# Kernel optimization log

Measured on AMD Instinct MI355X. Metric: run time of the kernel, lower is better.

Reference implementation:

```python
import jax, jax.numpy as jnp
import numpy as np

EPS = 1e-10


def setup_inputs() -> dict:
    key = jax.random.key(0)
    k1, k2 = jax.random.split(key)
    b, p, c = 8192, 512, 1000
    x = jax.random.normal(k1, (b, p), dtype=jnp.float32)
    means = jax.random.normal(k2, (c, p), dtype=jnp.float32)
    return {"x": x, "means": means}


def reference(x, means):
    # scale factor: L2 norm of the first class mean (np.linalg.norm(mean_logits_np[0]))
    scale = jnp.sqrt(jnp.sum(means[0] ** 2))
    # L2-normalize x along feature dim, then rescale to ||means[0]||
    xn = x / (jnp.linalg.norm(x, axis=1, keepdims=True) + EPS) * scale
    # logits = -||xn - mu_c||^2, expanded as -(||xn||^2 - 2 xn.mu + ||mu||^2)
    # avoids materializing the (b, num_classes, p) intermediate of the original
    x_sq = jnp.sum(xn * xn, axis=1, keepdims=True)          # (b, 1)
    m_sq = jnp.sum(means * means, axis=1)                   # (c,)
    cross = jnp.einsum('bp,cp->bc', xn, means)              # (b, c)
    logits = -(x_sq - 2.0 * cross + m_sq[None, :])
    return logits
```

## Files before the change

### kernel.cpp

```cpp
#include <hip/hip_runtime.h>
#include <hip/hip_bf16.h>
#include <stdint.h>

typedef __bf16 bf16x8 __attribute__((ext_vector_type(8)));
typedef float  f32x4  __attribute__((ext_vector_type(4)));
typedef __attribute__((address_space(1))) const void* gptr_t;
typedef __attribute__((address_space(3))) void*       sptr_t;

#define B_ROWS 8192
#define C_CLS  1000
#define C_PAD  1024
#define P_DIM  512
#define EPS    1e-10f

#define WS_MEANS_BF 0
#define WS_MSQ      1048576
#define WS_XN_BF    1052672
#define WS_XSQ      9441280

__global__ __launch_bounds__(64) void prep_means_k(const float* __restrict__ means,
                                                   __hip_bfloat16* __restrict__ means_bf,
                                                   float* __restrict__ m_sq) {
    const int c = blockIdx.x;
    const int l = threadIdx.x;
    if (c < C_CLS) {
        const float4* mr = (const float4*)(means + (size_t)c * P_DIM);
        float4 a = mr[l * 2];
        float4 b = mr[l * 2 + 1];
        float s = a.x * a.x + a.y * a.y + a.z * a.z + a.w * a.w
                + b.x * b.x + b.y * b.y + b.z * b.z + b.w * b.w;
        alignas(16) __hip_bfloat16 tmp[8];
        tmp[0] = __float2bfloat16(a.x); tmp[1] = __float2bfloat16(a.y);
        tmp[2] = __float2bfloat16(a.z); tmp[3] = __float2bfloat16(a.w);
        tmp[4] = __float2bfloat16(b.x); tmp[5] = __float2bfloat16(b.y);
        tmp[6] = __float2bfloat16(b.z); tmp[7] = __float2bfloat16(b.w);
        *(uint4*)(means_bf + (size_t)c * P_DIM + l * 8) = *(const uint4*)tmp;
        #pragma unroll
        for (int off = 32; off > 0; off >>= 1) s += __shfl_down(s, off);
        if (l == 0) m_sq[c] = s;
    } else {
        uint4 z = {0u, 0u, 0u, 0u};
        *(uint4*)(means_bf + (size_t)c * P_DIM + l * 8) = z;
        if (l == 0) m_sq[c] = 0.0f;
    }
}

__global__ __launch_bounds__(256) void prep_x_k(const float* __restrict__ x,
                                                const float* __restrict__ m_sq,
                                                __hip_bfloat16* __restrict__ xn_bf,
                                                float* __restrict__ x_sq) {
    const int w = threadIdx.x >> 6;
    const int l = threadIdx.x & 63;
    const int row = blockIdx.x * 4 + w;
    const float4* xr = (const float4*)(x + (size_t)row * P_DIM);
    float4 a = xr[l * 2];
    float4 b = xr[l * 2 + 1];
    float s = a.x * a.x + a.y * a.y + a.z * a.z + a.w * a.w
            + b.x * b.x + b.y * b.y + b.z * b.z + b.w * b.w;
    #pragma unroll
    for (int off = 32; off > 0; off >>= 1) s += __shfl_down(s, off);
    s = __shfl(s, 0);
    float norm  = sqrtf(s);
    float scale = sqrtf(m_sq[0]);
    float sc    = scale / (norm + EPS);
    alignas(16) __hip_bfloat16 tmp[8];
    tmp[0] = __float2bfloat16(a.x * sc); tmp[1] = __float2bfloat16(a.y * sc);
    tmp[2] = __float2bfloat16(a.z * sc); tmp[3] = __float2bfloat16(a.w * sc);
    tmp[4] = __float2bfloat16(b.x * sc); tmp[5] = __float2bfloat16(b.y * sc);
    tmp[6] = __float2bfloat16(b.z * sc); tmp[7] = __float2bfloat16(b.w * sc);
    *(uint4*)(xn_bf + (size_t)row * P_DIM + l * 8) = *(const uint4*)tmp;
    if (l == 0) {
        float sn = sc * norm;
        x_sq[row] = sn * sn;
    }
}

__global__ __launch_bounds__(256) void gemm_k(const __hip_bfloat16* __restrict__ A,
                                              const __hip_bfloat16* __restrict__ B,
                                              const float* __restrict__ x_sq,
                                              const float* __restrict__ m_sq,
                                              float* __restrict__ out) {
    __shared__ alignas(16) char lds[16384];
    const int t  = threadIdx.x;
    const int w  = t >> 6;
    const int l  = t & 63;
    const int wr = w >> 1;
    const int wc = w & 1;
    const int q   = l >> 4;
    const int m16 = l & 15;

    const int brow = blockIdx.y;
    const int bcol = blockIdx.x;

    f32x4 acc[4][4];
    #pragma unroll
    for (int i = 0; i < 4; ++i)
        #pragma unroll
        for (int j = 0; j < 4; ++j) {
            f32x4 z = {0.f, 0.f, 0.f, 0.f};
            acc[i][j] = z;
        }

    const char* Abase = (const char*)A + (size_t)(brow * 128) * (P_DIM * 2);
    const char* Bbase = (const char*)B + (size_t)(bcol * 128) * (P_DIM * 2);

    for (int k0 = 0; k0 < P_DIM; k0 += 32) {
        #pragma unroll
        for (int r = 0; r < 2; ++r) {
            const int o    = r * 4096 + t * 16;
            const int trow = o >> 6;
            const int kb   = o & 63;
            const char* gA = Abase + (size_t)trow * (P_DIM * 2) + k0 * 2 + kb;
            const char* gB = Bbase + (size_t)trow * (P_DIM * 2) + k0 * 2 + kb;
            char* dA = lds + r * 4096 + w * 1024;
            char* dB = lds + 8192 + r * 4096 + w * 1024;
            __builtin_amdgcn_global_load_lds((gptr_t)gA, (sptr_t)dA, 16, 0, 0);
            __builtin_amdgcn_global_load_lds((gptr_t)gB, (sptr_t)dB, 16, 0, 0);
        }
        __syncthreads();

        bf16x8 af[4], bfr[4];
        #pragma unroll
        for (int i = 0; i < 4; ++i) {
            const int m = wr * 64 + i * 16 + m16;
            af[i] = *(const bf16x8*)(lds + m * 64 + q * 16);
        }
        #pragma unroll
        for (int j = 0; j < 4; ++j) {
            const int n = wc * 64 + j * 16 + m16;
            bfr[j] = *(const bf16x8*)(lds + 8192 + n * 64 + q * 16);
        }
        #pragma unroll
        for (int i = 0; i < 4; ++i)
            #pragma unroll
            for (int j = 0; j < 4; ++j)
                acc[i][j] = __builtin_amdgcn_mfma_f32_16x16x32_bf16(af[i], bfr[j], acc[i][j], 0, 0, 0);
        __syncthreads();
    }

    const int rowbase = brow * 128 + wr * 64;
    const int colbase = bcol * 128 + wc * 64;
    float msq[4];
    #pragma unroll
    for (int j = 0; j < 4; ++j) {
        const int col = colbase + j * 16 + m16;
        msq[j] = (col < C_CLS) ? m_sq[col] : 0.0f;
    }
    #pragma unroll
    for (int i = 0; i < 4; ++i) {
        #pragma unroll
        for (int reg = 0; reg < 4; ++reg) {
            const int row = rowbase + i * 16 + q * 4 + reg;
            const float xsq = x_sq[row];
            #pragma unroll
            for (int j = 0; j < 4; ++j) {
                const int col = colbase + j * 16 + m16;
                if (col < C_CLS) {
                    out[(size_t)row * C_CLS + col] = 2.0f * acc[i][j][reg] - xsq - msq[j];
                }
            }
        }
    }
}

extern "C" void kernel_launch(void* const* d_in, const int* in_sizes, int n_in,
                              void* d_out, int out_size, void* d_ws, size_t ws_size,
                              hipStream_t stream) {
    const float* x     = (const float*)d_in[0];
    const float* means = (const float*)d_in[1];
    float* out = (float*)d_out;
    char* ws = (char*)d_ws;

    __hip_bfloat16* means_bf = (__hip_bfloat16*)(ws + WS_MEANS_BF);
    float*          m_sq     = (float*)(ws + WS_MSQ);
    __hip_bfloat16* xn_bf    = (__hip_bfloat16*)(ws + WS_XN_BF);
    float*          x_sq     = (float*)(ws + WS_XSQ);

    prep_means_k<<<C_PAD, 64, 0, stream>>>(means, means_bf, m_sq);
    prep_x_k<<<B_ROWS / 4, 256, 0, stream>>>(x, m_sq, xn_bf, x_sq);
    gemm_k<<<dim3(C_PAD / 128, B_ROWS / 128), 256, 0, stream>>>(xn_bf, means_bf, x_sq, m_sq, out);
}
```

Before: 98.28 us.

## Merge prep kernels and shrink GEMM tile to 64x128 for more blocks

Merges the two preprocessing kernels into one launch. Each x-row block recomputes the norm of means[0] itself, which removes the dependency on m_sq from the means pass. The GEMM tile shrinks from 128x128 to 64x128 with four waves each owning 64x32, and launch bounds request 4 blocks per CU, doubling the grid to 1024 blocks for better occupancy on the many-CU GPU. The cost is lower per-block data reuse (A tile shared over fewer columns) and redundant means[0] loads in every prep block.

```diff
diff --git a/kernel.cpp b/kernel.cpp
--- a/kernel.cpp
+++ b/kernel.cpp
@@ -18,131 +18,142 @@
 #define WS_XN_BF    1052672
 #define WS_XSQ      9441280
 
-__global__ __launch_bounds__(64) void prep_means_k(const float* __restrict__ means,
-                                                   __hip_bfloat16* __restrict__ means_bf,
-                                                   float* __restrict__ m_sq) {
-    const int c = blockIdx.x;
-    const int l = threadIdx.x;
-    if (c < C_CLS) {
-        const float4* mr = (const float4*)(means + (size_t)c * P_DIM);
-        float4 a = mr[l * 2];
-        float4 b = mr[l * 2 + 1];
-        float s = a.x * a.x + a.y * a.y + a.z * a.z + a.w * a.w
-                + b.x * b.x + b.y * b.y + b.z * b.z + b.w * b.w;
+__device__ __forceinline__ float dot8(float4 a, float4 b) {
+    return a.x * a.x + a.y * a.y + a.z * a.z + a.w * a.w
+         + b.x * b.x + b.y * b.y + b.z * b.z + b.w * b.w;
+}
+
+__global__ __launch_bounds__(256) void prep_k(const float* __restrict__ x,
+                                              const float* __restrict__ means,
+                                              __hip_bfloat16* __restrict__ means_bf,
+                                              float* __restrict__ m_sq,
+                                              __hip_bfloat16* __restrict__ xn_bf,
+                                              float* __restrict__ x_sq) {
+    const int w = threadIdx.x >> 6;
+    const int l = threadIdx.x & 63;
+    const int bid = blockIdx.x;
+
+    if (bid < B_ROWS / 4) {
+        const int row = bid * 4 + w;
+        const float4* m0 = (const float4*)means;
+        float4 ma = m0[l * 2];
+        float4 mb = m0[l * 2 + 1];
+        float ms = dot8(ma, mb);
+        const float4* xr = (const float4*)(x + (size_t)row * P_DIM);
+        float4 a = xr[l * 2];
+        float4 b = xr[l * 2 + 1];
+        float s = dot8(a, b);
+        #pragma unroll
+        for (int off = 32; off > 0; off >>= 1) {
+            ms += __shfl_down(ms, off);
+            s  += __shfl_down(s, off);
+        }
+        ms = __shfl(ms, 0);
+        s  = __shfl(s, 0);
+        float scale = sqrtf(ms);
+        float norm  = sqrtf(s);
+        float sc    = scale / (norm + EPS);
         alignas(16) __hip_bfloat16 tmp[8];
-        tmp[0] = __float2bfloat16(a.x); tmp[1] = __float2bfloat16(a.y);
-        tmp[2] = __float2bfloat16(a.z); tmp[3] = __float2bfloat16(a.w);
-        tmp[4] = __float2bfloat16(b.x); tmp[5] = __float2bfloat16(b.y);
-        tmp[6] = __float2bfloat16(b.z); tmp[7] = __float2bfloat16(b.w);
-        *(uint4*)(means_bf + (size_t)c * P_DIM + l * 8) = *(const uint4*)tmp;
-        #pragma unroll
-        for (int off = 32; off > 0; off >>= 1) s += __shfl_down(s, off);
-        if (l == 0) m_sq[c] = s;
+        tmp[0] = __float2bfloat16(a.x * sc); tmp[1] = __float2bfloat16(a.y * sc);
+        tmp[2] = __float2bfloat16(a.z * sc); tmp[3] = __float2bfloat16(a.w * sc);
+        tmp[4] = __float2bfloat16(b.x * sc); tmp[5] = __float2bfloat16(b.y * sc);
+        tmp[6] = __float2bfloat16(b.z * sc); tmp[7] = __float2bfloat16(b.w * sc);
+        *(uint4*)(xn_bf + (size_t)row * P_DIM + l * 8) = *(const uint4*)tmp;
+        if (l == 0) {
+            float sn = sc * norm;
+            x_sq[row] = sn * sn;
+        }
     } else {
-        uint4 z = {0u, 0u, 0u, 0u};
-        *(uint4*)(means_bf + (size_t)c * P_DIM + l * 8) = z;
-        if (l == 0) m_sq[c] = 0.0f;
+        const int c = (bid - B_ROWS / 4) * 4 + w;
+        if (c < C_CLS) {
+            const float4* mr = (const float4*)(means + (size_t)c * P_DIM);
+            float4 a = mr[l * 2];
+            float4 b = mr[l * 2 + 1];
+            float s = dot8(a, b);
+            alignas(16) __hip_bfloat16 tmp[8];
+            tmp[0] = __float2bfloat16(a.x); tmp[1] = __float2bfloat16(a.y);
+            tmp[2] = __float2bfloat16(a.z); tmp[3] = __float2bfloat16(a.w);
+            tmp[4] = __float2bfloat16(b.x); tmp[5] = __float2bfloat16(b.y);
+            tmp[6] = __float2bfloat16(b.z); tmp[7] = __float2bfloat16(b.w);
+            *(uint4*)(means_bf + (size_t)c * P_DIM + l * 8) = *(const uint4*)tmp;
+            #pragma unroll
+            for (int off = 32; off > 0; off >>= 1) s += __shfl_down(s, off);
+            if (l == 0) m_sq[c] = s;
+        } else {
+            uint4 z = {0u, 0u, 0u, 0u};
+            *(uint4*)(means_bf + (size_t)c * P_DIM + l * 8) = z;
+            if (l == 0) m_sq[c] = 0.0f;
+        }
     }
 }
 
-__global__ __launch_bounds__(256) void prep_x_k(const float* __restrict__ x,
-                                                const float* __restrict__ m_sq,
-                                                __hip_bfloat16* __restrict__ xn_bf,
-                                                float* __restrict__ x_sq) {
-    const int w = threadIdx.x >> 6;
-    const int l = threadIdx.x & 63;
-    const int row = blockIdx.x * 4 + w;
-    const float4* xr = (const float4*)(x + (size_t)row * P_DIM);
-    float4 a = xr[l * 2];
-    float4 b = xr[l * 2 + 1];
-    float s = a.x * a.x + a.y * a.y + a.z * a.z + a.w * a.w
-            + b.x * b.x + b.y * b.y + b.z * b.z + b.w * b.w;
-    #pragma unroll
-    for (int off = 32; off > 0; off >>= 1) s += __shfl_down(s, off);
-    s = __shfl(s, 0);
-    float norm  = sqrtf(s);
-    float scale = sqrtf(m_sq[0]);
-    float sc    = scale / (norm + EPS);
-    alignas(16) __hip_bfloat16 tmp[8];
-    tmp[0] = __float2bfloat16(a.x * sc); tmp[1] = __float2bfloat16(a.y * sc);
-    tmp[2] = __float2bfloat16(a.z * sc); tmp[3] = __float2bfloat16(a.w * sc);
-    tmp[4] = __float2bfloat16(b.x * sc); tmp[5] = __float2bfloat16(b.y * sc);
-    tmp[6] = __float2bfloat16(b.z * sc); tmp[7] = __float2bfloat16(b.w * sc);
-    *(uint4*)(xn_bf + (size_t)row * P_DIM + l * 8) = *(const uint4*)tmp;
-    if (l == 0) {
-        float sn = sc * norm;
-        x_sq[row] = sn * sn;
-    }
-}
-
-__global__ __launch_bounds__(256) void gemm_k(const __hip_bfloat16* __restrict__ A,
-                                              const __hip_bfloat16* __restrict__ B,
-                                              const float* __restrict__ x_sq,
-                                              const float* __restrict__ m_sq,
-                                              float* __restrict__ out) {
-    __shared__ alignas(16) char lds[16384];
-    const int t  = threadIdx.x;
-    const int w  = t >> 6;
-    const int l  = t & 63;
-    const int wr = w >> 1;
-    const int wc = w & 1;
+__global__ __launch_bounds__(256, 4) void gemm_k(const __hip_bfloat16* __restrict__ A,
+                                                 const __hip_bfloat16* __restrict__ B,
+                                                 const float* __restrict__ x_sq,
+                                                 const float* __restrict__ m_sq,
+                                                 float* __restrict__ out) {
+    __shared__ alignas(16) char lds[12288];
+    const int t   = threadIdx.x;
+    const int w   = t >> 6;
+    const int l   = t & 63;
     const int q   = l >> 4;
     const int m16 = l & 15;
 
     const int brow = blockIdx.y;
     const int bcol = blockIdx.x;
 
-    f32x4 acc[4][4];
+    f32x4 acc[4][2];
     #pragma unroll
     for (int i = 0; i < 4; ++i)
         #pragma unroll
-        for (int j = 0; j < 4; ++j) {
+        for (int j = 0; j < 2; ++j) {
             f32x4 z = {0.f, 0.f, 0.f, 0.f};
             acc[i][j] = z;
         }
 
-    const char* Abase = (const char*)A + (size_t)(brow * 128) * (P_DIM * 2);
+    const char* Abase = (const char*)A + (size_t)(brow * 64)  * (P_DIM * 2);
     const char* Bbase = (const char*)B + (size_t)(bcol * 128) * (P_DIM * 2);
 
     for (int k0 = 0; k0 < P_DIM; k0 += 32) {
         #pragma unroll
-        for (int r = 0; r < 2; ++r) {
-            const int o    = r * 4096 + t * 16;
-            const int trow = o >> 6;
-            const int kb   = o & 63;
-            const char* gA = Abase + (size_t)trow * (P_DIM * 2) + k0 * 2 + kb;
-            const char* gB = Bbase + (size_t)trow * (P_DIM * 2) + k0 * 2 + kb;
-            char* dA = lds + r * 4096 + w * 1024;
-            char* dB = lds + 8192 + r * 4096 + w * 1024;
-            __builtin_amdgcn_global_load_lds((gptr_t)gA, (sptr_t)dA, 16, 0, 0);
-            __builtin_amdgcn_global_load_lds((gptr_t)gB, (sptr_t)dB, 16, 0, 0);
+        for (int r = 0; r < 3; ++r) {
+            const int wbase = r * 4096 + w * 1024;
+            const int o     = wbase + l * 16;
+            const char* g;
+            if (r == 0) {
+                g = Abase + (size_t)(o >> 6) * (P_DIM * 2) + k0 * 2 + (o & 63);
+            } else {
+                const int o2 = o - 4096;
+                g = Bbase + (size_t)(o2 >> 6) * (P_DIM * 2) + k0 * 2 + (o2 & 63);
+            }
+            __builtin_amdgcn_global_load_lds((gptr_t)g, (sptr_t)(lds + wbase), 16, 0, 0);
         }
         __syncthreads();
 
-        bf16x8 af[4], bfr[4];
+        bf16x8 af[4], bfr[2];
         #pragma unroll
         for (int i = 0; i < 4; ++i) {
-            const int m = wr * 64 + i * 16 + m16;
+            const int m = i * 16 + m16;
             af[i] = *(const bf16x8*)(lds + m * 64 + q * 16);
         }
         #pragma unroll
-        for (int j = 0; j < 4; ++j) {
-            const int n = wc * 64 + j * 16 + m16;
-            bfr[j] = *(const bf16x8*)(lds + 8192 + n * 64 + q * 16);
+        for (int j = 0; j < 2; ++j) {
+            const int n = w * 32 + j * 16 + m16;
+            bfr[j] = *(const bf16x8*)(lds + 4096 + n * 64 + q * 16);
         }
         #pragma unroll
         for (int i = 0; i < 4; ++i)
             #pragma unroll
-            for (int j = 0; j < 4; ++j)
+            for (int j = 0; j < 2; ++j)
                 acc[i][j] = __builtin_amdgcn_mfma_f32_16x16x32_bf16(af[i], bfr[j], acc[i][j], 0, 0, 0);
         __syncthreads();
     }
 
-    const int rowbase = brow * 128 + wr * 64;
-    const int colbase = bcol * 128 + wc * 64;
-    float msq[4];
+    const int rowbase = brow * 64;
+    const int colbase = bcol * 128 + w * 32;
+    float msq[2];
     #pragma unroll
-    for (int j = 0; j < 4; ++j) {
+    for (int j = 0; j < 2; ++j) {
         const int col = colbase + j * 16 + m16;
         msq[j] = (col < C_CLS) ? m_sq[col] : 0.0f;
     }
@@ -153,7 +164,7 @@
             const int row = rowbase + i * 16 + q * 4 + reg;
             const float xsq = x_sq[row];
             #pragma unroll
-            for (int j = 0; j < 4; ++j) {
+            for (int j = 0; j < 2; ++j) {
                 const int col = colbase + j * 16 + m16;
                 if (col < C_CLS) {
                     out[(size_t)row * C_CLS + col] = 2.0f * acc[i][j][reg] - xsq - msq[j];
@@ -176,7 +187,6 @@
     __hip_bfloat16* xn_bf    = (__hip_bfloat16*)(ws + WS_XN_BF);
     float*          x_sq     = (float*)(ws + WS_XSQ);
 
-    prep_means_k<<<C_PAD, 64, 0, stream>>>(means, means_bf, m_sq);
-    prep_x_k<<<B_ROWS / 4, 256, 0, stream>>>(x, m_sq, xn_bf, x_sq);
-    gemm_k<<<dim3(C_PAD / 128, B_ROWS / 128), 256, 0, stream>>>(xn_bf, means_bf, x_sq, m_sq, out);
+    prep_k<<<B_ROWS / 4 + C_PAD / 4, 256, 0, stream>>>(x, means, means_bf, m_sq, xn_bf, x_sq);
+    gemm_k<<<dim3(C_PAD / 128, B_ROWS / 64), 256, 0, stream>>>(xn_bf, means_bf, x_sq, m_sq, out);
 }
```

New measurement: 95.48 us. -2.9%, faster.
